# Performance work log

Hardware: AMD Instinct MI355X
Metric: run time of the kernel (lower is better)

Reference implementation:

```python
import jax, jax.numpy as jnp
import numpy as np

N_NODES = 100000
N_EDGES = 1600000
IN_F = 128
HID = 128
OUT = 2


def setup_inputs() -> dict:
    key = jax.random.key(0)
    ks = jax.random.split(key, 12)
    s = lambda k, sh, f: jax.random.normal(k, sh, dtype=jnp.float32) * (1.0 / np.sqrt(f))
    return {
        "x": jax.random.normal(ks[0], (N_NODES, IN_F), dtype=jnp.float32),
        "W_self1": s(ks[1], (IN_F, HID), IN_F),
        "W_neigh1": s(ks[2], (IN_F, HID), IN_F),
        "b1": jnp.zeros((HID,), dtype=jnp.float32),
        "W_self2": s(ks[3], (HID, HID), HID),
        "W_neigh2": s(ks[4], (HID, HID), HID),
        "b2": jnp.zeros((HID,), dtype=jnp.float32),
        "W_final": s(ks[5], (HID, OUT), HID),
        "b_final": jnp.zeros((OUT,), dtype=jnp.float32),
        "src": jax.random.randint(ks[6], (N_EDGES,), 0, N_NODES, dtype=jnp.int32),
        "dst": jax.random.randint(ks[7], (N_EDGES,), 0, N_NODES, dtype=jnp.int32),
    }


def _sage_mean(x, src, dst, n_nodes, W_self, W_neigh, b):
    # gather neighbor (src) features, scatter-mean onto dst nodes
    msg_sum = jax.ops.segment_sum(x[src], dst, num_segments=n_nodes)  # [N, F]
    deg = jax.ops.segment_sum(jnp.ones((src.shape[0],), x.dtype), dst,
                              num_segments=n_nodes)  # [N]
    h_neigh = msg_sum / jnp.maximum(deg, 1.0)[:, None]
    # DGL SAGEConv(mean): fc_self(h_self) + fc_neigh(h_neigh) (+ bias)
    return x @ W_self + h_neigh @ W_neigh + b


def reference(x, W_self1, W_neigh1, b1, W_self2, W_neigh2, b2,
              W_final, b_final, src, dst):
    n = x.shape[0]
    h = jax.nn.relu(_sage_mean(x, src, dst, n, W_self1, W_neigh1, b1))
    h = jax.nn.relu(_sage_mean(h, src, dst, n, W_self2, W_neigh2, b2))
    return h @ W_final + b_final  # [N, 2]
```

## Files before the change

kernel.cpp:

```cpp
#include <hip/hip_runtime.h>

#define N_NODES 100000
#define N_EDGES 1600000
#define F 128

#define BSHIFT 11
#define BNODES 2048
#define NBUCK 49
#define P1_BLOCKS 128
#define P1_TPB 256
#define EPB1 (N_EDGES / P1_BLOCKS)
#define CAPB 384
#define P2_TPB 1024

typedef _Float16 f16x8 __attribute__((ext_vector_type(8)));
typedef _Float16 f16x4 __attribute__((ext_vector_type(4)));
typedef float f32x4 __attribute__((ext_vector_type(4)));

__global__ __launch_bounds__(P1_TPB) void k_part(const int* __restrict__ src,
                                                 const int* __restrict__ dst,
                                                 int2* __restrict__ stage,
                                                 int* __restrict__ pcnt) {
    __shared__ int cnt[NBUCK];
    int t = threadIdx.x, blk = blockIdx.x;
    if (t < NBUCK) cnt[t] = 0;
    __syncthreads();
    int base = blk * EPB1;
    for (int i = t; i < EPB1; i += P1_TPB) {
        int e = base + i;
        int s = src[e], d = dst[e];
        int b = d >> BSHIFT;
        int pos = atomicAdd(&cnt[b], 1);
        if (pos < CAPB) stage[((long)b * P1_BLOCKS + blk) * CAPB + pos] = make_int2(s, d);
    }
    __syncthreads();
    if (t < NBUCK) pcnt[t * P1_BLOCKS + blk] = min(cnt[t], CAPB);
}

__global__ void k_bucketsum(const int* __restrict__ pcnt, int* __restrict__ bbase,
                            int* __restrict__ row_start) {
    __shared__ int tot[64];
    int b = threadIdx.x;
    int s = 0;
    if (b < NBUCK)
        for (int i = 0; i < P1_BLOCKS; i++) s += pcnt[b * P1_BLOCKS + i];
    tot[b] = s;
    __syncthreads();
    if (b == 0) {
        int acc = 0;
        for (int i = 0; i < NBUCK; i++) {
            bbase[i] = acc;
            acc += tot[i];
        }
        bbase[NBUCK] = acc;
        row_start[N_NODES] = acc;
    }
}

__global__ __launch_bounds__(P2_TPB) void k_build(const int2* __restrict__ stage,
                                                  const int* __restrict__ pcnt,
                                                  const int* __restrict__ bbase,
                                                  int* __restrict__ row_start,
                                                  int* __restrict__ esrc) {
    __shared__ int cnt[BNODES];
    __shared__ int scanw[P2_TPB / 64];
    int b = blockIdx.x, t = threadIdx.x;
    int nodeBase = b << BSHIFT;
    for (int i = t; i < BNODES; i += P2_TPB) cnt[i] = 0;
    __syncthreads();
    int grp = t >> 8, gt = t & 255;
    for (int s = grp; s < P1_BLOCKS; s += 4) {
        int n = pcnt[b * P1_BLOCKS + s];
        const int2* seg = &stage[((long)b * P1_BLOCKS + s) * CAPB];
        for (int i = gt; i < n; i += 256) atomicAdd(&cnt[seg[i].y & (BNODES - 1)], 1);
    }
    __syncthreads();
    int c0 = cnt[2 * t], c1 = cnt[2 * t + 1];
    int v = c0 + c1;
    int lane = t & 63, wv = t >> 6;
    int x = v;
#pragma unroll
    for (int off = 1; off < 64; off <<= 1) {
        int y = __shfl_up(x, off, 64);
        if (lane >= off) x += y;
    }
    if (lane == 63) scanw[wv] = x;
    __syncthreads();
    if (t == 0) {
        int acc = 0;
        for (int i = 0; i < P2_TPB / 64; i++) {
            int y = scanw[i];
            scanw[i] = acc;
            acc += y;
        }
    }
    __syncthreads();
    int excl = x - v + scanw[wv];
    int base0 = bbase[b];
    int n0 = nodeBase + 2 * t;
    if (n0 < N_NODES) row_start[n0] = base0 + excl;
    if (n0 + 1 < N_NODES) row_start[n0 + 1] = base0 + excl + c0;
    cnt[2 * t] = excl;
    cnt[2 * t + 1] = excl + c0;
    __syncthreads();
    for (int s = grp; s < P1_BLOCKS; s += 4) {
        int n = pcnt[b * P1_BLOCKS + s];
        const int2* seg = &stage[((long)b * P1_BLOCKS + s) * CAPB];
        for (int i = gt; i < n; i += 256) {
            int2 p = seg[i];
            int pos = atomicAdd(&cnt[p.y & (BNODES - 1)], 1);
            esrc[base0 + pos] = p.x;
        }
    }
}

__global__ void k_cast(const float* __restrict__ x, _Float16* __restrict__ xh, int n4) {
    int i = blockIdx.x * blockDim.x + threadIdx.x;
    if (i < n4) {
        float4 v = ((const float4*)x)[i];
        f16x4 h;
        h.x = (_Float16)v.x; h.y = (_Float16)v.y;
        h.z = (_Float16)v.z; h.w = (_Float16)v.w;
        ((f16x4*)xh)[i] = h;
    }
}

__global__ void k_prepw(const float* __restrict__ Ws, const float* __restrict__ Wn,
                        _Float16* __restrict__ Wt) {
    int i = blockIdx.x * blockDim.x + threadIdx.x;
    int n = i >> 8;
    int k = i & 255;
    float v = (k < 128) ? Ws[k * F + n] : Wn[(k - 128) * F + n];
    Wt[n * 256 + k] = (_Float16)v;
}

__global__ __launch_bounds__(256) void k_agg(const f16x4* __restrict__ xf,
                                             const int* __restrict__ row_start,
                                             const int* __restrict__ esrc,
                                             f16x4* __restrict__ out) {
    int wave = (int)((blockIdx.x * blockDim.x + threadIdx.x) >> 6);
    int lane = threadIdx.x & 63;
    if (wave >= N_NODES) return;
    int sub = lane >> 5, col = lane & 31;
    int beg = row_start[wave], end = row_start[wave + 1];
    float ax = 0.f, ay = 0.f, az = 0.f, aw = 0.f;
    int j = beg;
    for (; j + 4 <= end; j += 4) {
        int e0 = esrc[j + sub], e1 = esrc[j + 2 + sub];
        f16x4 v0 = xf[(long)e0 * 32 + col];
        f16x4 v1 = xf[(long)e1 * 32 + col];
        ax += (float)v0.x + (float)v1.x;
        ay += (float)v0.y + (float)v1.y;
        az += (float)v0.z + (float)v1.z;
        aw += (float)v0.w + (float)v1.w;
    }
    for (; j < end; j += 2) {
        if (j + sub < end) {
            f16x4 v = xf[(long)esrc[j + sub] * 32 + col];
            ax += (float)v.x; ay += (float)v.y; az += (float)v.z; aw += (float)v.w;
        }
    }
    ax += __shfl_xor(ax, 32, 64);
    ay += __shfl_xor(ay, 32, 64);
    az += __shfl_xor(az, 32, 64);
    aw += __shfl_xor(aw, 32, 64);
    if (sub == 0) {
        float inv = (end > beg) ? 1.0f / (float)(end - beg) : 0.0f;
        f16x4 r;
        r.x = (_Float16)(ax * inv);
        r.y = (_Float16)(ay * inv);
        r.z = (_Float16)(az * inv);
        r.w = (_Float16)(aw * inv);
        out[(long)wave * 32 + col] = r;
    }
}

template <bool FINAL>
__global__ __launch_bounds__(256, 2) void k_gemm_mfma(
    const _Float16* __restrict__ Aself, const _Float16* __restrict__ Aneigh,
    const _Float16* __restrict__ Wt, const float* __restrict__ bias,
    _Float16* __restrict__ Hout, const float* __restrict__ Wf,
    const float* __restrict__ bf, float* __restrict__ Out) {
    const int M = N_NODES;
    __shared__ _Float16 Wl[4096 * 8];
    int w = threadIdx.x >> 6;
    int lane = threadIdx.x & 63;
    int q = lane >> 4;
    int ln = lane & 15;
    int rBase = blockIdx.x * 128 + w * 32;

#pragma unroll
    for (int i = 0; i < 16; i++) {
        int s = threadIdx.x + i * 256;
        int L = s & 63, ct = (s >> 6) & 7, ks = s >> 9;
        int g = (ct * 16 + (L & 15)) * 256 + ks * 32 + (L >> 4) * 8;
        *(f16x8*)&Wl[s * 8] = *(const f16x8*)&Wt[g];
    }

    f32x4 acc[2][8];
#pragma unroll
    for (int rt = 0; rt < 2; rt++)
#pragma unroll
        for (int ct = 0; ct < 8; ct++) acc[rt][ct] = (f32x4){0.f, 0.f, 0.f, 0.f};

    __syncthreads();

    for (int ks = 0; ks < 8; ks++) {
        const _Float16* Abase = (ks < 4) ? Aself : Aneigh;
        int k0 = (ks & 3) * 32;
        f16x8 b[8];
#pragma unroll
        for (int ct = 0; ct < 8; ct++)
            b[ct] = *(const f16x8*)&Wl[((ks * 8 + ct) * 64 + lane) * 8];
#pragma unroll
        for (int rt = 0; rt < 2; rt++) {
            int row = rBase + rt * 16 + ln;
            f16x8 a = {};
            if (row < M) a = *(const f16x8*)&Abase[(long)row * F + k0 + q * 8];
#pragma unroll
            for (int ct = 0; ct < 8; ct++)
                acc[rt][ct] = __builtin_amdgcn_mfma_f32_16x16x32_f16(a, b[ct], acc[rt][ct], 0, 0, 0);
        }
    }

    float bv[8];
#pragma unroll
    for (int ct = 0; ct < 8; ct++) bv[ct] = bias[ct * 16 + ln];

    if (!FINAL) {
#pragma unroll
        for (int rt = 0; rt < 2; rt++) {
#pragma unroll
            for (int r = 0; r < 4; r++) {
                int row = rBase + rt * 16 + q * 4 + r;
                if (row < M) {
#pragma unroll
                    for (int ct = 0; ct < 8; ct++) {
                        float h = acc[rt][ct][r] + bv[ct];
                        h = h > 0.f ? h : 0.f;
                        Hout[(long)row * F + ct * 16 + ln] = (_Float16)h;
                    }
                }
            }
        }
    } else {
        float wf0[8], wf1[8];
#pragma unroll
        for (int ct = 0; ct < 8; ct++) {
            int c = ct * 16 + ln;
            wf0[ct] = Wf[c * 2 + 0];
            wf1[ct] = Wf[c * 2 + 1];
        }
        float bf0 = bf[0], bf1 = bf[1];
#pragma unroll
        for (int rt = 0; rt < 2; rt++) {
#pragma unroll
            for (int r = 0; r < 4; r++) {
                int row = rBase + rt * 16 + q * 4 + r;
                float p0 = 0.f, p1 = 0.f;
#pragma unroll
                for (int ct = 0; ct < 8; ct++) {
                    float h = acc[rt][ct][r] + bv[ct];
                    h = h > 0.f ? h : 0.f;
                    p0 += h * wf0[ct];
                    p1 += h * wf1[ct];
                }
#pragma unroll
                for (int off = 1; off < 16; off <<= 1) {
                    p0 += __shfl_xor(p0, off, 64);
                    p1 += __shfl_xor(p1, off, 64);
                }
                if (ln == 0 && row < M) {
                    Out[(long)row * 2 + 0] = p0 + bf0;
                    Out[(long)row * 2 + 1] = p1 + bf1;
                }
            }
        }
    }
}

extern "C" void kernel_launch(void* const* d_in, const int* in_sizes, int n_in,
                              void* d_out, int out_size, void* d_ws, size_t ws_size,
                              hipStream_t stream) {
    const float* x   = (const float*)d_in[0];
    const float* Ws1 = (const float*)d_in[1];
    const float* Wn1 = (const float*)d_in[2];
    const float* b1  = (const float*)d_in[3];
    const float* Ws2 = (const float*)d_in[4];
    const float* Wn2 = (const float*)d_in[5];
    const float* b2  = (const float*)d_in[6];
    const float* Wf  = (const float*)d_in[7];
    const float* bf  = (const float*)d_in[8];
    const int* src   = (const int*)d_in[9];
    const int* dst   = (const int*)d_in[10];
    float* out = (float*)d_out;

    char* ws = (char*)d_ws;
    int*      row_start = (int*)(ws + 0);
    int*      bbase     = (int*)(ws + 400016);
    int*      pcnt      = (int*)(ws + 400272);
    int2*     stage     = (int2*)(ws + 425360);
    int*      esrc      = (int*)(ws + 19692944);
    _Float16* xh        = (_Float16*)(ws + 26092944);
    _Float16* hneigh    = (_Float16*)(ws + 51692944);
    _Float16* h1        = (_Float16*)(ws + 77292944);
    _Float16* Wt1       = (_Float16*)(ws + 102892944);
    _Float16* Wt2       = (_Float16*)(ws + 102958480);

    const int TPB = 256;
    k_part<<<P1_BLOCKS, P1_TPB, 0, stream>>>(src, dst, stage, pcnt);
    k_bucketsum<<<1, 64, 0, stream>>>(pcnt, bbase, row_start);
    k_build<<<NBUCK, P2_TPB, 0, stream>>>(stage, pcnt, bbase, row_start, esrc);

    k_cast<<<(N_NODES * F / 4 + TPB - 1) / TPB, TPB, 0, stream>>>(x, xh, N_NODES * F / 4);
    k_prepw<<<128, 256, 0, stream>>>(Ws1, Wn1, Wt1);
    k_prepw<<<128, 256, 0, stream>>>(Ws2, Wn2, Wt2);

    k_agg<<<(N_NODES + 3) / 4, 256, 0, stream>>>((const f16x4*)xh, row_start, esrc,
                                                 (f16x4*)hneigh);
    k_gemm_mfma<false><<<(N_NODES + 127) / 128, 256, 0, stream>>>(
        xh, hneigh, Wt1, b1, h1, nullptr, nullptr, nullptr);
    k_agg<<<(N_NODES + 3) / 4, 256, 0, stream>>>((const f16x4*)h1, row_start, esrc,
                                                 (f16x4*)hneigh);
    k_gemm_mfma<true><<<(N_NODES + 127) / 128, 256, 0, stream>>>(
        h1, hneigh, Wt2, b2, nullptr, Wf, bf, out);
}
```

Measured before the change: 443.5 us.

## Sort CSR neighbors by source range, merge weight prep, unroll aggregation

The CSR build kernel now makes 13 passes over the staged edges and on each pass inserts only the edges whose source falls in one 8192-node range. Within each destination row the neighbors therefore come out roughly sorted by source, which is meant to improve cache locality of the feature gathers in aggregation. The two weight-prep launches are merged into one kernel, and the aggregation loop gains an 8-edge unrolled body for more loads in flight. The price is rereading the staged edges 13 times, with a block barrier after each pass, inside the build kernel.

```diff
diff --git a/kernel.cpp b/kernel.cpp
--- a/kernel.cpp
+++ b/kernel.cpp
@@ -12,6 +12,8 @@
 #define EPB1 (N_EDGES / P1_BLOCKS)
 #define CAPB 384
 #define P2_TPB 1024
+#define SRC_SHIFT 13
+#define NSPASS 13
 
 typedef _Float16 f16x8 __attribute__((ext_vector_type(8)));
 typedef _Float16 f16x4 __attribute__((ext_vector_type(4)));
@@ -103,14 +105,19 @@
     cnt[2 * t] = excl;
     cnt[2 * t + 1] = excl + c0;
     __syncthreads();
-    for (int s = grp; s < P1_BLOCKS; s += 4) {
-        int n = pcnt[b * P1_BLOCKS + s];
-        const int2* seg = &stage[((long)b * P1_BLOCKS + s) * CAPB];
-        for (int i = gt; i < n; i += 256) {
-            int2 p = seg[i];
-            int pos = atomicAdd(&cnt[p.y & (BNODES - 1)], 1);
-            esrc[base0 + pos] = p.x;
-        }
+    for (int p = 0; p < NSPASS; p++) {
+        for (int s = grp; s < P1_BLOCKS; s += 4) {
+            int n = pcnt[b * P1_BLOCKS + s];
+            const int2* seg = &stage[((long)b * P1_BLOCKS + s) * CAPB];
+            for (int i = gt; i < n; i += 256) {
+                int2 pr = seg[i];
+                if ((pr.x >> SRC_SHIFT) == p) {
+                    int pos = atomicAdd(&cnt[pr.y & (BNODES - 1)], 1);
+                    esrc[base0 + pos] = pr.x;
+                }
+            }
+        }
+        __syncthreads();
     }
 }
 
@@ -125,11 +132,17 @@
     }
 }
 
-__global__ void k_prepw(const float* __restrict__ Ws, const float* __restrict__ Wn,
-                        _Float16* __restrict__ Wt) {
+__global__ void k_prepw(const float* __restrict__ Ws1, const float* __restrict__ Wn1,
+                        const float* __restrict__ Ws2, const float* __restrict__ Wn2,
+                        _Float16* __restrict__ Wt1, _Float16* __restrict__ Wt2) {
     int i = blockIdx.x * blockDim.x + threadIdx.x;
-    int n = i >> 8;
-    int k = i & 255;
+    int which = i >> 15;
+    int j = i & 32767;
+    int n = j >> 8;
+    int k = j & 255;
+    const float* Ws = which ? Ws2 : Ws1;
+    const float* Wn = which ? Wn2 : Wn1;
+    _Float16* Wt = which ? Wt2 : Wt1;
     float v = (k < 128) ? Ws[k * F + n] : Wn[(k - 128) * F + n];
     Wt[n * 256 + k] = (_Float16)v;
 }
@@ -145,6 +158,18 @@
     int beg = row_start[wave], end = row_start[wave + 1];
     float ax = 0.f, ay = 0.f, az = 0.f, aw = 0.f;
     int j = beg;
+    for (; j + 8 <= end; j += 8) {
+        int e0 = esrc[j + sub], e1 = esrc[j + 2 + sub];
+        int e2 = esrc[j + 4 + sub], e3 = esrc[j + 6 + sub];
+        f16x4 v0 = xf[(long)e0 * 32 + col];
+        f16x4 v1 = xf[(long)e1 * 32 + col];
+        f16x4 v2 = xf[(long)e2 * 32 + col];
+        f16x4 v3 = xf[(long)e3 * 32 + col];
+        ax += (float)v0.x + (float)v1.x + (float)v2.x + (float)v3.x;
+        ay += (float)v0.y + (float)v1.y + (float)v2.y + (float)v3.y;
+        az += (float)v0.z + (float)v1.z + (float)v2.z + (float)v3.z;
+        aw += (float)v0.w + (float)v1.w + (float)v2.w + (float)v3.w;
+    }
     for (; j + 4 <= end; j += 4) {
         int e0 = esrc[j + sub], e1 = esrc[j + 2 + sub];
         f16x4 v0 = xf[(long)e0 * 32 + col];
@@ -313,8 +338,7 @@
     k_build<<<NBUCK, P2_TPB, 0, stream>>>(stage, pcnt, bbase, row_start, esrc);
 
     k_cast<<<(N_NODES * F / 4 + TPB - 1) / TPB, TPB, 0, stream>>>(x, xh, N_NODES * F / 4);
-    k_prepw<<<128, 256, 0, stream>>>(Ws1, Wn1, Wt1);
-    k_prepw<<<128, 256, 0, stream>>>(Ws2, Wn2, Wt2);
+    k_prepw<<<256, 256, 0, stream>>>(Ws1, Wn1, Ws2, Wn2, Wt1, Wt2);
 
     k_agg<<<(N_NODES + 3) / 4, 256, 0, stream>>>((const f16x4*)xh, row_start, esrc,
                                                  (f16x4*)hneigh);
```

After: 653.4 us. 47.4% more time.
